# Optimization experiments

Measured on AMD Instinct MI355X. Metric: run time of the kernel, lower is better.

## Reference

```python
import jax, jax.numpy as jnp
import numpy as np

NEG_INF = -jnp.inf


def setup_inputs() -> dict:
    key = jax.random.key(0)
    x = jax.random.normal(key, (512, 1024, 192), dtype=jnp.float32)
    return {"x": x, "kept_number": 256}


def reference(x, kept_number):
    # x: [B, N, C]; literal translation of the given Merge.forward (eval mode)
    B, N, C = x.shape
    if B <= kept_number:  # original checks x.shape[0]
        return x
    metric = jax.lax.stop_gradient(x)
    # original: metric / metric.norm(dim=1, keepdim=True)  -> norm over token dim
    metric = metric / jnp.linalg.norm(metric, axis=1, keepdims=True)
    unimp = metric[:, kept_number:]              # [B, N-k, C]
    compress_number = unimp.shape[0]             # == B (as in source)
    imp = metric[:, :kept_number]                # [B, k, C]
    sim = jnp.einsum('buc,bkc->buk', unimp, imp)  # [B, N-k, k]
    sim = sim.at[:, :, 0].set(NEG_INF)           # class_token=True
    node_idx = jnp.argmax(sim, axis=-1)          # [B, N-k], first-max like torch
    dst_idx = node_idx[:, :compress_number]      # [B, B]
    src = x[:, kept_number:][:, :compress_number]  # [B, B, C] (rows actually scattered)
    dst = x[:, :kept_number]                     # [B, k, C]
    # scatter_reduce(-2, reduce='mean', include_self=True):
    # out = (dst + sum of scattered src) / (1 + count)
    sums = jax.vmap(lambda i, s: jnp.zeros((kept_number, C), x.dtype).at[i].add(s))(dst_idx, src)
    counts = jax.vmap(lambda i: jnp.zeros((kept_number,), x.dtype).at[i].add(jnp.asarray(1, x.dtype)))(dst_idx)
    return (dst + sums) / (counts[:, :, None] + 1)
```

## Files before the change

kernel.cpp:

```cpp
#include <hip/hip_runtime.h>
#include <hip/hip_bf16.h>
#include <math.h>

#define Nn   1024
#define Cn   192
#define KEPT 256
#define COMP 512
#define UT   128
#define KT   64
#define MARGIN 4e-4f
#define WCAP 1024

typedef __attribute__((ext_vector_type(8))) _Float16 half8v;
typedef __attribute__((ext_vector_type(4))) float f32x4;

__device__ __forceinline__ unsigned encf(float f) {
    unsigned u = __float_as_uint(f);
    return (u & 0x80000000u) ? ~u : (u | 0x80000000u);
}
__device__ __forceinline__ unsigned long long cvt4(float m0, float m1, float m2, float m3) {
    unsigned short h0 = __builtin_bit_cast(unsigned short, (_Float16)m0);
    unsigned short h1 = __builtin_bit_cast(unsigned short, (_Float16)m1);
    unsigned short h2 = __builtin_bit_cast(unsigned short, (_Float16)m2);
    unsigned short h3 = __builtin_bit_cast(unsigned short, (_Float16)m3);
    return (unsigned long long)h0 | ((unsigned long long)h1 << 16)
         | ((unsigned long long)h2 << 32) | ((unsigned long long)h3 << 48);
}

__global__ __launch_bounds__(768) void norm_kernel(const float* __restrict__ x,
                                                   float* __restrict__ w,
                                                   float* __restrict__ rsw) {
    __shared__ float4 red[16][48];
    int b = blockIdx.x, t = threadIdx.x;
    int c4 = t % 48, ng = t / 48;
    const float* xb = x + (size_t)b * Nn * Cn;
    float4 s = make_float4(0.f, 0.f, 0.f, 0.f);
    for (int i = 0; i < 64; ++i) {
        float4 v = *reinterpret_cast<const float4*>(
            xb + (size_t)(ng * 64 + i) * Cn + c4 * 4);
        s.x += v.x * v.x; s.y += v.y * v.y; s.z += v.z * v.z; s.w += v.w * v.w;
    }
    red[ng][c4] = s;
    __syncthreads();
    if (t < 48) {
        float4 a = make_float4(0.f, 0.f, 0.f, 0.f);
        #pragma unroll
        for (int g = 0; g < 16; ++g) {
            float4 v = red[g][t];
            a.x += v.x; a.y += v.y; a.z += v.z; a.w += v.w;
        }
        float4 wv = make_float4(1.0f / a.x, 1.0f / a.y, 1.0f / a.z, 1.0f / a.w);
        float4 rv = make_float4(rsqrtf(a.x), rsqrtf(a.y), rsqrtf(a.z), rsqrtf(a.w));
        *reinterpret_cast<float4*>(w   + (size_t)b * Cn + t * 4) = wv;
        *reinterpret_cast<float4*>(rsw + (size_t)b * Cn + t * 4) = rv;
    }
}

__global__ __launch_bounds__(512) void sim_kernel(const float* __restrict__ x,
                                                  const float* __restrict__ w,
                                                  const float* __restrict__ rsw,
                                                  int* __restrict__ dst_idx) {
    __shared__ __align__(16) unsigned short su_h[UT * Cn];
    __shared__ __align__(16) unsigned short sk_h[KT * Cn];
    __shared__ float rl[Cn];
    __shared__ float wl[Cn];
    __shared__ float rowthr[UT];
    __shared__ unsigned long long best[UT];
    __shared__ unsigned short wlist[WCAP];
    __shared__ int nc;

    const int bi   = blockIdx.x;
    const int xcd  = bi & 7;
    const int slot = bi >> 3;
    const int b    = xcd * 64 + (slot >> 2);
    const int u0   = (slot & 3) * UT;
    const int t    = threadIdx.x;
    const float* xb = x + (size_t)b * Nn * Cn;

    if (t < Cn) { rl[t] = rsw[b * Cn + t]; wl[t] = w[b * Cn + t]; }
    if (t < UT) { rowthr[t] = INFINITY; best[t] = 0ull; }
    if (t == 0) nc = 0;
    __syncthreads();

    #pragma unroll
    for (int i = 0; i < 12; ++i) {
        int idx = t + 512 * i;
        int r = idx / 48, c4 = idx % 48;
        float4 v = *reinterpret_cast<const float4*>(
            xb + (size_t)(KEPT + u0 + r) * Cn + c4 * 4);
        unsigned long long h = cvt4(v.x * rl[c4 * 4 + 0], v.y * rl[c4 * 4 + 1],
                                    v.z * rl[c4 * 4 + 2], v.w * rl[c4 * 4 + 3]);
        int byte = r * 384 + ((c4 * 8) ^ ((r & 7) << 4));
        *reinterpret_cast<unsigned long long*>(reinterpret_cast<char*>(su_h) + byte) = h;
    }

    float4 pf[6];
    #pragma unroll
    for (int i = 0; i < 6; ++i) {
        int idx = t + 512 * i;
        int r = idx / 48, c4 = idx % 48;
        pf[i] = *reinterpret_cast<const float4*>(xb + (size_t)r * Cn + c4 * 4);
    }

    const int wv   = t >> 6;
    const int ln   = t & 63;
    const int l15  = ln & 15;
    const int hi2  = ln >> 4;
    const int akey = (l15 & 7) << 4;
    const int abase = (wv * 16 + l15) * 384;
    int bbase[4];
    #pragma unroll
    for (int j = 0; j < 4; ++j) bbase[j] = (j * 16 + l15) * 384;

    f32x4 acc[4][4];
    #pragma unroll
    for (int kt = 0; kt < 4; ++kt)
        #pragma unroll
        for (int j = 0; j < 4; ++j) acc[kt][j] = (f32x4)0.f;

    #pragma unroll
    for (int kt = 0; kt < 4; ++kt) {
        __syncthreads();
        #pragma unroll
        for (int i = 0; i < 6; ++i) {
            int idx = t + 512 * i;
            int r = idx / 48, c4 = idx % 48;
            unsigned long long h = cvt4(pf[i].x * rl[c4 * 4 + 0], pf[i].y * rl[c4 * 4 + 1],
                                        pf[i].z * rl[c4 * 4 + 2], pf[i].w * rl[c4 * 4 + 3]);
            int byte = r * 384 + ((c4 * 8) ^ ((r & 7) << 4));
            *reinterpret_cast<unsigned long long*>(reinterpret_cast<char*>(sk_h) + byte) = h;
        }
        __syncthreads();
        if (kt < 3) {
            #pragma unroll
            for (int i = 0; i < 6; ++i) {
                int idx = t + 512 * i;
                int r = idx / 48, c4 = idx % 48;
                pf[i] = *reinterpret_cast<const float4*>(
                    xb + (size_t)((kt + 1) * KT + r) * Cn + c4 * 4);
            }
        }

        #pragma unroll
        for (int ks = 0; ks < 6; ++ks) {
            int koff = (ks * 64 + hi2 * 16) ^ akey;
            half8v ah = *reinterpret_cast<const half8v*>(
                reinterpret_cast<const char*>(su_h) + abase + koff);
            #pragma unroll
            for (int j = 0; j < 4; ++j) {
                half8v bh = *reinterpret_cast<const half8v*>(
                    reinterpret_cast<const char*>(sk_h) + bbase[j] + koff);
                acc[kt][j] = __builtin_amdgcn_mfma_f32_16x16x32_f16(ah, bh, acc[kt][j], 0, 0, 0);
            }
        }
    }

    float v1[4], v2[4];
    int   i1[4];
    #pragma unroll
    for (int r = 0; r < 4; ++r) { v1[r] = -INFINITY; v2[r] = -INFINITY; i1[r] = 1; }

    #pragma unroll
    for (int kt = 0; kt < 4; ++kt)
        #pragma unroll
        for (int j = 0; j < 4; ++j) {
            int k = kt * KT + j * 16 + l15;
            #pragma unroll
            for (int r = 0; r < 4; ++r) {
                float v = acc[kt][j][r];
                if (k != 0) {
                    if (v > v1[r]) { v2[r] = v1[r]; v1[r] = v; i1[r] = k; }
                    else if (v > v2[r]) v2[r] = v;
                }
            }
        }

    #pragma unroll
    for (int r = 0; r < 4; ++r) {
        #pragma unroll
        for (int off = 1; off < 16; off <<= 1) {
            float ov1 = __shfl_xor(v1[r], off);
            int   oi1 = __shfl_xor(i1[r], off);
            float ov2 = __shfl_xor(v2[r], off);
            if (ov1 > v1[r] || (ov1 == v1[r] && oi1 < i1[r])) {
                v2[r] = fmaxf(v1[r], ov2);
                v1[r] = ov1; i1[r] = oi1;
            } else {
                v2[r] = fmaxf(v2[r], ov1);
            }
        }
    }

    if (l15 == 0) {
        #pragma unroll
        for (int r = 0; r < 4; ++r) {
            int ur = wv * 16 + hi2 * 4 + r;
            if (v1[r] - v2[r] > MARGIN) dst_idx[b * COMP + u0 + ur] = i1[r];
            else rowthr[ur] = v1[r] - MARGIN;
        }
    }
    __syncthreads();

    #pragma unroll
    for (int kt = 0; kt < 4; ++kt)
        #pragma unroll
        for (int j = 0; j < 4; ++j) {
            int k = kt * KT + j * 16 + l15;
            if (k == 0) continue;
            #pragma unroll
            for (int r = 0; r < 4; ++r) {
                int ur = wv * 16 + hi2 * 4 + r;
                if (acc[kt][j][r] >= rowthr[ur]) {
                    int pos = atomicAdd(&nc, 1);
                    if (pos < WCAP)
                        wlist[pos] = (unsigned short)((ur << 8) | k);
                }
            }
        }
    __syncthreads();

    int n = nc < WCAP ? nc : WCAP;
    for (int ci = wv; ci < n; ci += 8) {
        unsigned item = wlist[ci];
        int ur = item >> 8, k = item & 255;
        const float* xu = xb + (size_t)(KEPT + u0 + ur) * Cn;
        const float* xk = xb + (size_t)k * Cn;
        float p = 0.f;
        if (ln < 48) {
            float4 a  = *reinterpret_cast<const float4*>(xu + ln * 4);
            float4 b4 = *reinterpret_cast<const float4*>(xk + ln * 4);
            p = a.x * b4.x * wl[ln * 4 + 0] + a.y * b4.y * wl[ln * 4 + 1]
              + a.z * b4.z * wl[ln * 4 + 2] + a.w * b4.w * wl[ln * 4 + 3];
        }
        #pragma unroll
        for (int off = 32; off >= 1; off >>= 1) p += __shfl_xor(p, off);
        if (ln == 0) {
            unsigned long long e = ((unsigned long long)encf(p) << 32)
                                 | (unsigned long long)(0xFFFFFFFFu - (unsigned)k);
            atomicMax(&best[ur], e);
        }
    }
    __syncthreads();

    if (t < UT && rowthr[t] < 3.0e38f) {
        unsigned k = 0xFFFFFFFFu - (unsigned)(best[t] & 0xFFFFFFFFull);
        dst_idx[b * COMP + u0 + t] = (int)k;
    }
}

__global__ __launch_bounds__(512) void merge_kernel(const float* __restrict__ x,
                                                    const int* __restrict__ dst_idx,
                                                    float* __restrict__ out) {
    __shared__ int sidx[COMP];
    __shared__ int cnt[KEPT];
    __shared__ int off[KEPT];
    __shared__ int fill[KEPT];
    __shared__ unsigned short list[COMP];

    int b = blockIdx.x, t = threadIdx.x;

    if (t < KEPT) { cnt[t] = 0; fill[t] = 0; }
    sidx[t] = dst_idx[b * COMP + t];
    __syncthreads();
    atomicAdd(&cnt[sidx[t]], 1);
    __syncthreads();

    if (t < KEPT) off[t] = cnt[t];
    __syncthreads();
    #pragma unroll
    for (int d = 1; d < KEPT; d <<= 1) {
        int v = 0;
        if (t < KEPT && t >= d) v = off[t - d];
        __syncthreads();
        if (t < KEPT) off[t] += v;
        __syncthreads();
    }

    {
        int k = sidx[t];
        int pos = off[k] - cnt[k] + atomicAdd(&fill[k], 1);
        list[pos] = (unsigned short)t;
    }
    __syncthreads();

    const float* xb   = x   + (size_t)b * Nn * Cn;
    float*       outb = out + (size_t)b * KEPT * Cn;
    const int wv  = t >> 6, ln = t & 63;
    const int qtr = ln >> 4;
    const int cq  = ln & 15;

    for (int pass = 0; pass < 8; ++pass) {
        int k = pass * 32 + wv * 4 + qtr;
        int e = off[k], c = cnt[k], s0 = e - c;
        const float* xr = xb + (size_t)k * Cn;
        float4 a0 = *reinterpret_cast<const float4*>(xr + cq * 4);
        float4 a1 = *reinterpret_cast<const float4*>(xr + (cq + 16) * 4);
        float4 a2 = *reinterpret_cast<const float4*>(xr + (cq + 32) * 4);
        for (int i = s0; i < e; ++i) {
            const float* xs = xb + (size_t)(KEPT + list[i]) * Cn;
            float4 v0  = *reinterpret_cast<const float4*>(xs + cq * 4);
            float4 v1v = *reinterpret_cast<const float4*>(xs + (cq + 16) * 4);
            float4 v2v = *reinterpret_cast<const float4*>(xs + (cq + 32) * 4);
            a0.x += v0.x;  a0.y += v0.y;  a0.z += v0.z;  a0.w += v0.w;
            a1.x += v1v.x; a1.y += v1v.y; a1.z += v1v.z; a1.w += v1v.w;
            a2.x += v2v.x; a2.y += v2v.y; a2.z += v2v.z; a2.w += v2v.w;
        }
        float rc = 1.0f / ((float)c + 1.0f);
        float* orow = outb + (size_t)k * Cn;
        *reinterpret_cast<float4*>(orow + cq * 4) =
            make_float4(a0.x * rc, a0.y * rc, a0.z * rc, a0.w * rc);
        *reinterpret_cast<float4*>(orow + (cq + 16) * 4) =
            make_float4(a1.x * rc, a1.y * rc, a1.z * rc, a1.w * rc);
        *reinterpret_cast<float4*>(orow + (cq + 32) * 4) =
            make_float4(a2.x * rc, a2.y * rc, a2.z * rc, a2.w * rc);
    }
}

extern "C" void kernel_launch(void* const* d_in, const int* in_sizes, int n_in,
                              void* d_out, int out_size, void* d_ws, size_t ws_size,
                              hipStream_t stream) {
    const float* x = (const float*)d_in[0];
    float* out = (float*)d_out;

    char* ws = (char*)d_ws;
    float* w       = (float*)ws;
    float* rsw     = (float*)(ws + (size_t)512 * Cn * 4);
    int*   dst_idx = (int*)  (ws + (size_t)2 * 512 * Cn * 4);

    norm_kernel<<<dim3(512), dim3(768), 0, stream>>>(x, w, rsw);
    sim_kernel<<<dim3(2048), dim3(512), 0, stream>>>(x, w, rsw, dst_idx);
    merge_kernel<<<dim3(512), dim3(512), 0, stream>>>(x, dst_idx, out);
}
```

Baseline: 251.5 us.

## Fuse similarity argmax and merge into one per-batch kernel

The similarity/argmax kernel and the merge kernel are combined into a single kernel with one block per batch. That block loops over the four 128-row u-chunks, keeps dst indices in shared memory instead of global, and reuses the sk_h buffer for the merge's count, offset and list arrays. This removes a kernel launch and the dst_idx round trip through global memory. In exchange the grid drops from 2048 blocks to 512, which cuts parallelism and removes the XCD-aware block mapping, and WCAP is halved, so more rows could overflow the candidate list.

New measurement: 435.6 us. 1.73x slower.

```diff
diff --git a/kernel.cpp b/kernel.cpp
--- a/kernel.cpp
+++ b/kernel.cpp
@@ -9,7 +9,7 @@
 #define UT   128
 #define KT   64
 #define MARGIN 4e-4f
-#define WCAP 1024
+#define WCAP 512
 
 typedef __attribute__((ext_vector_type(8))) _Float16 half8v;
 typedef __attribute__((ext_vector_type(4))) float f32x4;
@@ -56,10 +56,10 @@
     }
 }
 
-__global__ __launch_bounds__(512) void sim_kernel(const float* __restrict__ x,
-                                                  const float* __restrict__ w,
-                                                  const float* __restrict__ rsw,
-                                                  int* __restrict__ dst_idx) {
+__global__ __launch_bounds__(512, 4) void simmerge_kernel(const float* __restrict__ x,
+                                                          const float* __restrict__ w,
+                                                          const float* __restrict__ rsw,
+                                                          float* __restrict__ out) {
     __shared__ __align__(16) unsigned short su_h[UT * Cn];
     __shared__ __align__(16) unsigned short sk_h[KT * Cn];
     __shared__ float rl[Cn];
@@ -68,39 +68,14 @@
     __shared__ unsigned long long best[UT];
     __shared__ unsigned short wlist[WCAP];
     __shared__ int nc;
-
-    const int bi   = blockIdx.x;
-    const int xcd  = bi & 7;
-    const int slot = bi >> 3;
-    const int b    = xcd * 64 + (slot >> 2);
-    const int u0   = (slot & 3) * UT;
-    const int t    = threadIdx.x;
+    __shared__ unsigned short dstl[COMP];
+
+    const int b = blockIdx.x;
+    const int t = threadIdx.x;
     const float* xb = x + (size_t)b * Nn * Cn;
 
     if (t < Cn) { rl[t] = rsw[b * Cn + t]; wl[t] = w[b * Cn + t]; }
-    if (t < UT) { rowthr[t] = INFINITY; best[t] = 0ull; }
-    if (t == 0) nc = 0;
-    __syncthreads();
-
-    #pragma unroll
-    for (int i = 0; i < 12; ++i) {
-        int idx = t + 512 * i;
-        int r = idx / 48, c4 = idx % 48;
-        float4 v = *reinterpret_cast<const float4*>(
-            xb + (size_t)(KEPT + u0 + r) * Cn + c4 * 4);
-        unsigned long long h = cvt4(v.x * rl[c4 * 4 + 0], v.y * rl[c4 * 4 + 1],
-                                    v.z * rl[c4 * 4 + 2], v.w * rl[c4 * 4 + 3]);
-        int byte = r * 384 + ((c4 * 8) ^ ((r & 7) << 4));
-        *reinterpret_cast<unsigned long long*>(reinterpret_cast<char*>(su_h) + byte) = h;
-    }
-
-    float4 pf[6];
-    #pragma unroll
-    for (int i = 0; i < 6; ++i) {
-        int idx = t + 512 * i;
-        int r = idx / 48, c4 = idx % 48;
-        pf[i] = *reinterpret_cast<const float4*>(xb + (size_t)r * Cn + c4 * 4);
-    }
+    __syncthreads();
 
     const int wv   = t >> 6;
     const int ln   = t & 63;
@@ -112,186 +87,205 @@
     #pragma unroll
     for (int j = 0; j < 4; ++j) bbase[j] = (j * 16 + l15) * 384;
 
-    f32x4 acc[4][4];
-    #pragma unroll
-    for (int kt = 0; kt < 4; ++kt)
-        #pragma unroll
-        for (int j = 0; j < 4; ++j) acc[kt][j] = (f32x4)0.f;
-
-    #pragma unroll
-    for (int kt = 0; kt < 4; ++kt) {
-        __syncthreads();
+    for (int uc = 0; uc < 4; ++uc) {
+        const int u0 = uc * UT;
+        __syncthreads();
+        if (t < UT) { rowthr[t] = INFINITY; best[t] = 0ull; }
+        if (t == 0) nc = 0;
+        __syncthreads();
+
+        #pragma unroll
+        for (int i = 0; i < 12; ++i) {
+            int idx = t + 512 * i;
+            int r = idx / 48, c4 = idx % 48;
+            float4 v = *reinterpret_cast<const float4*>(
+                xb + (size_t)(KEPT + u0 + r) * Cn + c4 * 4);
+            unsigned long long h = cvt4(v.x * rl[c4 * 4 + 0], v.y * rl[c4 * 4 + 1],
+                                        v.z * rl[c4 * 4 + 2], v.w * rl[c4 * 4 + 3]);
+            int byte = r * 384 + ((c4 * 8) ^ ((r & 7) << 4));
+            *reinterpret_cast<unsigned long long*>(reinterpret_cast<char*>(su_h) + byte) = h;
+        }
+
+        float4 pf[6];
         #pragma unroll
         for (int i = 0; i < 6; ++i) {
             int idx = t + 512 * i;
             int r = idx / 48, c4 = idx % 48;
-            unsigned long long h = cvt4(pf[i].x * rl[c4 * 4 + 0], pf[i].y * rl[c4 * 4 + 1],
-                                        pf[i].z * rl[c4 * 4 + 2], pf[i].w * rl[c4 * 4 + 3]);
-            int byte = r * 384 + ((c4 * 8) ^ ((r & 7) << 4));
-            *reinterpret_cast<unsigned long long*>(reinterpret_cast<char*>(sk_h) + byte) = h;
-        }
-        __syncthreads();
-        if (kt < 3) {
+            pf[i] = *reinterpret_cast<const float4*>(xb + (size_t)r * Cn + c4 * 4);
+        }
+
+        f32x4 acc[4][4];
+        #pragma unroll
+        for (int kt = 0; kt < 4; ++kt)
+            #pragma unroll
+            for (int j = 0; j < 4; ++j) acc[kt][j] = (f32x4)0.f;
+
+        #pragma unroll
+        for (int kt = 0; kt < 4; ++kt) {
+            __syncthreads();
             #pragma unroll
             for (int i = 0; i < 6; ++i) {
                 int idx = t + 512 * i;
                 int r = idx / 48, c4 = idx % 48;
-                pf[i] = *reinterpret_cast<const float4*>(
-                    xb + (size_t)((kt + 1) * KT + r) * Cn + c4 * 4);
-            }
-        }
-
-        #pragma unroll
-        for (int ks = 0; ks < 6; ++ks) {
-            int koff = (ks * 64 + hi2 * 16) ^ akey;
-            half8v ah = *reinterpret_cast<const half8v*>(
-                reinterpret_cast<const char*>(su_h) + abase + koff);
+                unsigned long long h = cvt4(pf[i].x * rl[c4 * 4 + 0], pf[i].y * rl[c4 * 4 + 1],
+                                            pf[i].z * rl[c4 * 4 + 2], pf[i].w * rl[c4 * 4 + 3]);
+                int byte = r * 384 + ((c4 * 8) ^ ((r & 7) << 4));
+                *reinterpret_cast<unsigned long long*>(reinterpret_cast<char*>(sk_h) + byte) = h;
+            }
+            __syncthreads();
+            if (kt < 3) {
+                #pragma unroll
+                for (int i = 0; i < 6; ++i) {
+                    int idx = t + 512 * i;
+                    int r = idx / 48, c4 = idx % 48;
+                    pf[i] = *reinterpret_cast<const float4*>(
+                        xb + (size_t)((kt + 1) * KT + r) * Cn + c4 * 4);
+                }
+            }
+
+            #pragma unroll
+            for (int ks = 0; ks < 6; ++ks) {
+                int koff = (ks * 64 + hi2 * 16) ^ akey;
+                half8v ah = *reinterpret_cast<const half8v*>(
+                    reinterpret_cast<const char*>(su_h) + abase + koff);
+                #pragma unroll
+                for (int j = 0; j < 4; ++j) {
+                    half8v bh = *reinterpret_cast<const half8v*>(
+                        reinterpret_cast<const char*>(sk_h) + bbase[j] + koff);
+                    acc[kt][j] = __builtin_amdgcn_mfma_f32_16x16x32_f16(ah, bh, acc[kt][j], 0, 0, 0);
+                }
+            }
+        }
+
+        float v1[4], v2[4];
+        int   i1[4];
+        #pragma unroll
+        for (int r = 0; r < 4; ++r) { v1[r] = -INFINITY; v2[r] = -INFINITY; i1[r] = 1; }
+
+        #pragma unroll
+        for (int kt = 0; kt < 4; ++kt)
             #pragma unroll
             for (int j = 0; j < 4; ++j) {
-                half8v bh = *reinterpret_cast<const half8v*>(
-                    reinterpret_cast<const char*>(sk_h) + bbase[j] + koff);
-                acc[kt][j] = __builtin_amdgcn_mfma_f32_16x16x32_f16(ah, bh, acc[kt][j], 0, 0, 0);
-            }
-        }
-    }
-
-    float v1[4], v2[4];
-    int   i1[4];
-    #pragma unroll
-    for (int r = 0; r < 4; ++r) { v1[r] = -INFINITY; v2[r] = -INFINITY; i1[r] = 1; }
-
-    #pragma unroll
-    for (int kt = 0; kt < 4; ++kt)
-        #pragma unroll
-        for (int j = 0; j < 4; ++j) {
-            int k = kt * KT + j * 16 + l15;
-            #pragma unroll
-            for (int r = 0; r < 4; ++r) {
-                float v = acc[kt][j][r];
-                if (k != 0) {
-                    if (v > v1[r]) { v2[r] = v1[r]; v1[r] = v; i1[r] = k; }
-                    else if (v > v2[r]) v2[r] = v;
-                }
-            }
-        }
-
-    #pragma unroll
-    for (int r = 0; r < 4; ++r) {
-        #pragma unroll
-        for (int off = 1; off < 16; off <<= 1) {
-            float ov1 = __shfl_xor(v1[r], off);
-            int   oi1 = __shfl_xor(i1[r], off);
-            float ov2 = __shfl_xor(v2[r], off);
-            if (ov1 > v1[r] || (ov1 == v1[r] && oi1 < i1[r])) {
-                v2[r] = fmaxf(v1[r], ov2);
-                v1[r] = ov1; i1[r] = oi1;
-            } else {
-                v2[r] = fmaxf(v2[r], ov1);
-            }
-        }
-    }
-
-    if (l15 == 0) {
+                int k = kt * KT + j * 16 + l15;
+                #pragma unroll
+                for (int r = 0; r < 4; ++r) {
+                    float v = acc[kt][j][r];
+                    if (k != 0) {
+                        if (v > v1[r]) { v2[r] = v1[r]; v1[r] = v; i1[r] = k; }
+                        else if (v > v2[r]) v2[r] = v;
+                    }
+                }
+            }
+
         #pragma unroll
         for (int r = 0; r < 4; ++r) {
-            int ur = wv * 16 + hi2 * 4 + r;
-            if (v1[r] - v2[r] > MARGIN) dst_idx[b * COMP + u0 + ur] = i1[r];
-            else rowthr[ur] = v1[r] - MARGIN;
-        }
-    }
-    __syncthreads();
-
-    #pragma unroll
-    for (int kt = 0; kt < 4; ++kt)
-        #pragma unroll
-        for (int j = 0; j < 4; ++j) {
-            int k = kt * KT + j * 16 + l15;
-            if (k == 0) continue;
+            #pragma unroll
+            for (int off = 1; off < 16; off <<= 1) {
+                float ov1 = __shfl_xor(v1[r], off);
+                int   oi1 = __shfl_xor(i1[r], off);
+                float ov2 = __shfl_xor(v2[r], off);
+                if (ov1 > v1[r] || (ov1 == v1[r] && oi1 < i1[r])) {
+                    v2[r] = fmaxf(v1[r], ov2);
+                    v1[r] = ov1; i1[r] = oi1;
+                } else {
+                    v2[r] = fmaxf(v2[r], ov1);
+                }
+            }
+        }
+
+        if (l15 == 0) {
             #pragma unroll
             for (int r = 0; r < 4; ++r) {
                 int ur = wv * 16 + hi2 * 4 + r;
-                if (acc[kt][j][r] >= rowthr[ur]) {
-                    int pos = atomicAdd(&nc, 1);
-                    if (pos < WCAP)
-                        wlist[pos] = (unsigned short)((ur << 8) | k);
-                }
-            }
-        }
-    __syncthreads();
-
-    int n = nc < WCAP ? nc : WCAP;
-    for (int ci = wv; ci < n; ci += 8) {
-        unsigned item = wlist[ci];
-        int ur = item >> 8, k = item & 255;
-        const float* xu = xb + (size_t)(KEPT + u0 + ur) * Cn;
-        const float* xk = xb + (size_t)k * Cn;
-        float p = 0.f;
-        if (ln < 48) {
-            float4 a  = *reinterpret_cast<const float4*>(xu + ln * 4);
-            float4 b4 = *reinterpret_cast<const float4*>(xk + ln * 4);
-            p = a.x * b4.x * wl[ln * 4 + 0] + a.y * b4.y * wl[ln * 4 + 1]
-              + a.z * b4.z * wl[ln * 4 + 2] + a.w * b4.w * wl[ln * 4 + 3];
-        }
-        #pragma unroll
-        for (int off = 32; off >= 1; off >>= 1) p += __shfl_xor(p, off);
-        if (ln == 0) {
-            unsigned long long e = ((unsigned long long)encf(p) << 32)
-                                 | (unsigned long long)(0xFFFFFFFFu - (unsigned)k);
-            atomicMax(&best[ur], e);
-        }
-    }
-    __syncthreads();
-
-    if (t < UT && rowthr[t] < 3.0e38f) {
-        unsigned k = 0xFFFFFFFFu - (unsigned)(best[t] & 0xFFFFFFFFull);
-        dst_idx[b * COMP + u0 + t] = (int)k;
-    }
-}
-
-__global__ __launch_bounds__(512) void merge_kernel(const float* __restrict__ x,
-                                                    const int* __restrict__ dst_idx,
-                                                    float* __restrict__ out) {
-    __shared__ int sidx[COMP];
-    __shared__ int cnt[KEPT];
-    __shared__ int off[KEPT];
-    __shared__ int fill[KEPT];
-    __shared__ unsigned short list[COMP];
-
-    int b = blockIdx.x, t = threadIdx.x;
+                if (v1[r] - v2[r] > MARGIN) dstl[u0 + ur] = (unsigned short)i1[r];
+                else rowthr[ur] = v1[r] - MARGIN;
+            }
+        }
+        __syncthreads();
+
+        #pragma unroll
+        for (int kt = 0; kt < 4; ++kt)
+            #pragma unroll
+            for (int j = 0; j < 4; ++j) {
+                int k = kt * KT + j * 16 + l15;
+                if (k == 0) continue;
+                #pragma unroll
+                for (int r = 0; r < 4; ++r) {
+                    int ur = wv * 16 + hi2 * 4 + r;
+                    if (acc[kt][j][r] >= rowthr[ur]) {
+                        int pos = atomicAdd(&nc, 1);
+                        if (pos < WCAP)
+                            wlist[pos] = (unsigned short)((ur << 8) | k);
+                    }
+                }
+            }
+        __syncthreads();
+
+        int n = nc < WCAP ? nc : WCAP;
+        for (int ci = wv; ci < n; ci += 8) {
+            unsigned item = wlist[ci];
+            int ur = item >> 8, k = item & 255;
+            const float* xu = xb + (size_t)(KEPT + u0 + ur) * Cn;
+            const float* xk = xb + (size_t)k * Cn;
+            float p = 0.f;
+            if (ln < 48) {
+                float4 a  = *reinterpret_cast<const float4*>(xu + ln * 4);
+                float4 b4 = *reinterpret_cast<const float4*>(xk + ln * 4);
+                p = a.x * b4.x * wl[ln * 4 + 0] + a.y * b4.y * wl[ln * 4 + 1]
+                  + a.z * b4.z * wl[ln * 4 + 2] + a.w * b4.w * wl[ln * 4 + 3];
+            }
+            #pragma unroll
+            for (int off = 32; off >= 1; off >>= 1) p += __shfl_xor(p, off);
+            if (ln == 0) {
+                unsigned long long e = ((unsigned long long)encf(p) << 32)
+                                     | (unsigned long long)(0xFFFFFFFFu - (unsigned)k);
+                atomicMax(&best[ur], e);
+            }
+        }
+        __syncthreads();
+
+        if (t < UT && rowthr[t] < 3.0e38f) {
+            unsigned k = 0xFFFFFFFFu - (unsigned)(best[t] & 0xFFFFFFFFull);
+            dstl[u0 + t] = (unsigned short)k;
+        }
+    }
+    __syncthreads();
+
+    int* cnt  = reinterpret_cast<int*>(sk_h);
+    int* offp = cnt + KEPT;
+    int* fill = offp + KEPT;
+    unsigned short* list = reinterpret_cast<unsigned short*>(fill + KEPT);
 
     if (t < KEPT) { cnt[t] = 0; fill[t] = 0; }
-    sidx[t] = dst_idx[b * COMP + t];
-    __syncthreads();
-    atomicAdd(&cnt[sidx[t]], 1);
-    __syncthreads();
-
-    if (t < KEPT) off[t] = cnt[t];
+    __syncthreads();
+    atomicAdd(&cnt[dstl[t]], 1);
+    __syncthreads();
+
+    if (t < KEPT) offp[t] = cnt[t];
     __syncthreads();
     #pragma unroll
     for (int d = 1; d < KEPT; d <<= 1) {
         int v = 0;
-        if (t < KEPT && t >= d) v = off[t - d];
-        __syncthreads();
-        if (t < KEPT) off[t] += v;
+        if (t < KEPT && t >= d) v = offp[t - d];
+        __syncthreads();
+        if (t < KEPT) offp[t] += v;
         __syncthreads();
     }
 
     {
-        int k = sidx[t];
-        int pos = off[k] - cnt[k] + atomicAdd(&fill[k], 1);
+        int k = dstl[t];
+        int pos = offp[k] - cnt[k] + atomicAdd(&fill[k], 1);
         list[pos] = (unsigned short)t;
     }
     __syncthreads();
 
-    const float* xb   = x   + (size_t)b * Nn * Cn;
-    float*       outb = out + (size_t)b * KEPT * Cn;
-    const int wv  = t >> 6, ln = t & 63;
+    float* outb = out + (size_t)b * KEPT * Cn;
     const int qtr = ln >> 4;
     const int cq  = ln & 15;
 
     for (int pass = 0; pass < 8; ++pass) {
         int k = pass * 32 + wv * 4 + qtr;
-        int e = off[k], c = cnt[k], s0 = e - c;
+        int e = offp[k], c = cnt[k], s0 = e - c;
         const float* xr = xb + (size_t)k * Cn;
         float4 a0 = *reinterpret_cast<const float4*>(xr + cq * 4);
         float4 a1 = *reinterpret_cast<const float4*>(xr + (cq + 16) * 4);
@@ -323,11 +317,9 @@
     float* out = (float*)d_out;
 
     char* ws = (char*)d_ws;
-    float* w       = (float*)ws;
-    float* rsw     = (float*)(ws + (size_t)512 * Cn * 4);
-    int*   dst_idx = (int*)  (ws + (size_t)2 * 512 * Cn * 4);
+    float* w   = (float*)ws;
+    float* rsw = (float*)(ws + (size_t)512 * Cn * 4);
 
     norm_kernel<<<dim3(512), dim3(768), 0, stream>>>(x, w, rsw);
-    sim_kernel<<<dim3(2048), dim3(512), 0, stream>>>(x, w, rsw, dst_idx);
-    merge_kernel<<<dim3(512), dim3(512), 0, stream>>>(x, dst_idx, out);
-}
+    simmerge_kernel<<<dim3(512), dim3(512), 0, stream>>>(x, w, rsw, out);
+}
```

## Keep A fragments in registers, shrink sim tiles to raise occupancy

Applied to the files above, without the earlier changes.

The sim kernel now handles 64 unimportant rows per block with 256 threads instead of 128 rows with 512 threads, and launches twice as many blocks. Each wave loads its A operand straight from global memory into registers as fp16 fragments, so the shared-memory A tile is gone. The kept-token tile shrinks to 32 rows with 8 iterations and no register prefetch, which cuts shared memory so more blocks can be resident (launch_bounds 256,3). The cost is that the kept tokens are reloaded and converted twice as often across blocks, global loads are no longer overlapped with MFMA work, and the smaller tie-candidate list could overflow.

New measurement: 329.0 us. 30.8% more time.

```diff
diff --git a/kernel.cpp b/kernel.cpp
--- a/kernel.cpp
+++ b/kernel.cpp
@@ -6,10 +6,10 @@
 #define Cn   192
 #define KEPT 256
 #define COMP 512
-#define UT   128
-#define KT   64
+#define UCH  64
+#define KT   32
 #define MARGIN 4e-4f
-#define WCAP 1024
+#define WCAP 256
 
 typedef __attribute__((ext_vector_type(8))) _Float16 half8v;
 typedef __attribute__((ext_vector_type(4))) float f32x4;
@@ -56,101 +56,91 @@
     }
 }
 
-__global__ __launch_bounds__(512) void sim_kernel(const float* __restrict__ x,
-                                                  const float* __restrict__ w,
-                                                  const float* __restrict__ rsw,
-                                                  int* __restrict__ dst_idx) {
-    __shared__ __align__(16) unsigned short su_h[UT * Cn];
+__global__ __launch_bounds__(256, 3) void sim_kernel(const float* __restrict__ x,
+                                                     const float* __restrict__ w,
+                                                     const float* __restrict__ rsw,
+                                                     int* __restrict__ dst_idx) {
     __shared__ __align__(16) unsigned short sk_h[KT * Cn];
     __shared__ float rl[Cn];
     __shared__ float wl[Cn];
-    __shared__ float rowthr[UT];
-    __shared__ unsigned long long best[UT];
+    __shared__ float rowthr[UCH];
+    __shared__ unsigned long long best[UCH];
     __shared__ unsigned short wlist[WCAP];
     __shared__ int nc;
 
     const int bi   = blockIdx.x;
     const int xcd  = bi & 7;
     const int slot = bi >> 3;
-    const int b    = xcd * 64 + (slot >> 2);
-    const int u0   = (slot & 3) * UT;
+    const int b    = xcd * 64 + (slot >> 3);
+    const int u0   = (slot & 7) * UCH;
     const int t    = threadIdx.x;
     const float* xb = x + (size_t)b * Nn * Cn;
 
     if (t < Cn) { rl[t] = rsw[b * Cn + t]; wl[t] = w[b * Cn + t]; }
-    if (t < UT) { rowthr[t] = INFINITY; best[t] = 0ull; }
+    if (t < UCH) { rowthr[t] = INFINITY; best[t] = 0ull; }
     if (t == 0) nc = 0;
     __syncthreads();
-
-    #pragma unroll
-    for (int i = 0; i < 12; ++i) {
-        int idx = t + 512 * i;
-        int r = idx / 48, c4 = idx % 48;
-        float4 v = *reinterpret_cast<const float4*>(
-            xb + (size_t)(KEPT + u0 + r) * Cn + c4 * 4);
-        unsigned long long h = cvt4(v.x * rl[c4 * 4 + 0], v.y * rl[c4 * 4 + 1],
-                                    v.z * rl[c4 * 4 + 2], v.w * rl[c4 * 4 + 3]);
-        int byte = r * 384 + ((c4 * 8) ^ ((r & 7) << 4));
-        *reinterpret_cast<unsigned long long*>(reinterpret_cast<char*>(su_h) + byte) = h;
-    }
-
-    float4 pf[6];
-    #pragma unroll
-    for (int i = 0; i < 6; ++i) {
-        int idx = t + 512 * i;
-        int r = idx / 48, c4 = idx % 48;
-        pf[i] = *reinterpret_cast<const float4*>(xb + (size_t)r * Cn + c4 * 4);
-    }
 
     const int wv   = t >> 6;
     const int ln   = t & 63;
     const int l15  = ln & 15;
     const int hi2  = ln >> 4;
     const int akey = (l15 & 7) << 4;
-    const int abase = (wv * 16 + l15) * 384;
-    int bbase[4];
-    #pragma unroll
-    for (int j = 0; j < 4; ++j) bbase[j] = (j * 16 + l15) * 384;
-
-    f32x4 acc[4][4];
-    #pragma unroll
-    for (int kt = 0; kt < 4; ++kt)
-        #pragma unroll
-        for (int j = 0; j < 4; ++j) acc[kt][j] = (f32x4)0.f;
-
-    #pragma unroll
-    for (int kt = 0; kt < 4; ++kt) {
+    int bbase[2];
+    #pragma unroll
+    for (int j = 0; j < 2; ++j) bbase[j] = (j * 16 + l15) * 384;
+
+    half8v af[6];
+    {
+        const float* arow = xb + (size_t)(KEPT + u0 + wv * 16 + l15) * Cn;
+        #pragma unroll
+        for (int ks = 0; ks < 6; ++ks) {
+            int c0 = ks * 32 + hi2 * 8;
+            float4 v0 = *reinterpret_cast<const float4*>(arow + c0);
+            float4 v1 = *reinterpret_cast<const float4*>(arow + c0 + 4);
+            half8v a;
+            a[0] = (_Float16)(v0.x * rl[c0 + 0]);
+            a[1] = (_Float16)(v0.y * rl[c0 + 1]);
+            a[2] = (_Float16)(v0.z * rl[c0 + 2]);
+            a[3] = (_Float16)(v0.w * rl[c0 + 3]);
+            a[4] = (_Float16)(v1.x * rl[c0 + 4]);
+            a[5] = (_Float16)(v1.y * rl[c0 + 5]);
+            a[6] = (_Float16)(v1.z * rl[c0 + 6]);
+            a[7] = (_Float16)(v1.w * rl[c0 + 7]);
+            af[ks] = a;
+        }
+    }
+
+    f32x4 acc[8][2];
+    #pragma unroll
+    for (int kt = 0; kt < 8; ++kt)
+        #pragma unroll
+        for (int j = 0; j < 2; ++j) acc[kt][j] = (f32x4)0.f;
+
+    #pragma unroll
+    for (int kt = 0; kt < 8; ++kt) {
         __syncthreads();
         #pragma unroll
         for (int i = 0; i < 6; ++i) {
-            int idx = t + 512 * i;
+            int idx = t + 256 * i;
             int r = idx / 48, c4 = idx % 48;
-            unsigned long long h = cvt4(pf[i].x * rl[c4 * 4 + 0], pf[i].y * rl[c4 * 4 + 1],
-                                        pf[i].z * rl[c4 * 4 + 2], pf[i].w * rl[c4 * 4 + 3]);
+            float4 v = *reinterpret_cast<const float4*>(
+                xb + (size_t)(kt * KT + r) * Cn + c4 * 4);
+            unsigned long long h = cvt4(v.x * rl[c4 * 4 + 0], v.y * rl[c4 * 4 + 1],
+                                        v.z * rl[c4 * 4 + 2], v.w * rl[c4 * 4 + 3]);
             int byte = r * 384 + ((c4 * 8) ^ ((r & 7) << 4));
             *reinterpret_cast<unsigned long long*>(reinterpret_cast<char*>(sk_h) + byte) = h;
         }
         __syncthreads();
-        if (kt < 3) {
-            #pragma unroll
-            for (int i = 0; i < 6; ++i) {
-                int idx = t + 512 * i;
-                int r = idx / 48, c4 = idx % 48;
-                pf[i] = *reinterpret_cast<const float4*>(
-                    xb + (size_t)((kt + 1) * KT + r) * Cn + c4 * 4);
-            }
-        }
 
         #pragma unroll
         for (int ks = 0; ks < 6; ++ks) {
             int koff = (ks * 64 + hi2 * 16) ^ akey;
-            half8v ah = *reinterpret_cast<const half8v*>(
-                reinterpret_cast<const char*>(su_h) + abase + koff);
             #pragma unroll
-            for (int j = 0; j < 4; ++j) {
+            for (int j = 0; j < 2; ++j) {
                 half8v bh = *reinterpret_cast<const half8v*>(
                     reinterpret_cast<const char*>(sk_h) + bbase[j] + koff);
-                acc[kt][j] = __builtin_amdgcn_mfma_f32_16x16x32_f16(ah, bh, acc[kt][j], 0, 0, 0);
+                acc[kt][j] = __builtin_amdgcn_mfma_f32_16x16x32_f16(af[ks], bh, acc[kt][j], 0, 0, 0);
             }
         }
     }
@@ -161,9 +151,9 @@
     for (int r = 0; r < 4; ++r) { v1[r] = -INFINITY; v2[r] = -INFINITY; i1[r] = 1; }
 
     #pragma unroll
-    for (int kt = 0; kt < 4; ++kt)
-        #pragma unroll
-        for (int j = 0; j < 4; ++j) {
+    for (int kt = 0; kt < 8; ++kt)
+        #pragma unroll
+        for (int j = 0; j < 2; ++j) {
             int k = kt * KT + j * 16 + l15;
             #pragma unroll
             for (int r = 0; r < 4; ++r) {
@@ -202,9 +192,9 @@
     __syncthreads();
 
     #pragma unroll
-    for (int kt = 0; kt < 4; ++kt)
-        #pragma unroll
-        for (int j = 0; j < 4; ++j) {
+    for (int kt = 0; kt < 8; ++kt)
+        #pragma unroll
+        for (int j = 0; j < 2; ++j) {
             int k = kt * KT + j * 16 + l15;
             if (k == 0) continue;
             #pragma unroll
@@ -220,7 +210,7 @@
     __syncthreads();
 
     int n = nc < WCAP ? nc : WCAP;
-    for (int ci = wv; ci < n; ci += 8) {
+    for (int ci = wv; ci < n; ci += 4) {
         unsigned item = wlist[ci];
         int ur = item >> 8, k = item & 255;
         const float* xu = xb + (size_t)(KEPT + u0 + ur) * Cn;
@@ -242,7 +232,7 @@
     }
     __syncthreads();
 
-    if (t < UT && rowthr[t] < 3.0e38f) {
+    if (t < UCH && rowthr[t] < 3.0e38f) {
         unsigned k = 0xFFFFFFFFu - (unsigned)(best[t] & 0xFFFFFFFFull);
         dst_idx[b * COMP + u0 + t] = (int)k;
     }
@@ -328,6 +318,6 @@
     int*   dst_idx = (int*)  (ws + (size_t)2 * 512 * Cn * 4);
 
     norm_kernel<<<dim3(512), dim3(768), 0, stream>>>(x, w, rsw);
-    sim_kernel<<<dim3(2048), dim3(512), 0, stream>>>(x, w, rsw, dst_idx);
+    sim_kernel<<<dim3(4096), dim3(256), 0, stream>>>(x, w, rsw, dst_idx);
     merge_kernel<<<dim3(512), dim3(512), 0, stream>>>(x, dst_idx, out);
 }
```
